# Performance work log

Measured on AMD Instinct MI355X. Metric: run time of the kernel, lower is better.

The kernel has to match this reference:

```python
import jax, jax.numpy as jnp
import numpy as np

N_NODES = 50000
EMB = 256
HEADS = 2
N_BASE_EDGES = 100000


def setup_inputs() -> dict:
    key = jax.random.key(0)
    ks = jax.random.split(key, 12)
    x = jax.random.normal(ks[0], (N_NODES, EMB), dtype=jnp.float32)
    # bipartite edges: sources in left half, targets in right half -> no self-loops
    src = jax.random.randint(ks[1], (N_BASE_EDGES,), 0, N_NODES // 2)
    dst = jax.random.randint(ks[2], (N_BASE_EDGES,), N_NODES // 2, N_NODES)
    edge_index = jnp.stack([src, dst]).astype(jnp.int64)
    hd = EMB // HEADS
    s = 0.02
    params = {
        "Wkqv": jax.random.normal(ks[3], (EMB, 3 * EMB), dtype=jnp.float32) * s,
        "bkqv": jnp.zeros((3 * EMB,), dtype=jnp.float32),
        "W1": jax.random.normal(ks[4], (2 * hd, hd), dtype=jnp.float32) * s,
        "b1": jnp.zeros((hd,), dtype=jnp.float32),
        "W2": jax.random.normal(ks[5], (hd, 1), dtype=jnp.float32) * s,
        "b2": jnp.zeros((1,), dtype=jnp.float32),
        "Wout": jax.random.normal(ks[6], (EMB, EMB), dtype=jnp.float32) * s,
        "bout": jnp.zeros((EMB,), dtype=jnp.float32),
    }
    return {"x": x, "edge_index": edge_index, **params}


def reference(x, edge_index, Wkqv, bkqv, W1, b1, W2, b2, Wout, bout):
    N, emb = x.shape
    H = HEADS
    hd = emb // H
    # MetaGNNNoEdgeAttr.forward preprocessing: make undirected + self loops.
    # Input is bipartite (no self-loops), so remove_self_loops is a no-op.
    ei = jnp.concatenate([edge_index, edge_index[::-1]], axis=1)
    loops = jnp.arange(N, dtype=edge_index.dtype)
    src = jnp.concatenate([ei[0], loops])  # j (message source)
    dst = jnp.concatenate([ei[1], loops])  # i (message target / softmax index)

    # single GNN layer (n_layers=1)
    kqv = x @ Wkqv + bkqv  # [N, 3*emb]
    q = kqv[dst, :emb].reshape(-1, H, hd)                                  # [E,H,hd]
    k = kqv[src, emb:2 * emb].reshape(-1, H, hd) / jnp.sqrt(jnp.float32(hd))
    v = kqv[src, 2 * emb:].reshape(-1, H, hd)

    h = jax.nn.relu(jnp.concatenate([k, q], axis=-1) @ W1 + b1)  # [E,H,hd]
    a = (h @ W2 + b2).squeeze(-1)                                # [E,H]

    # segment softmax over destination nodes (every node has a self-loop)
    m = jax.ops.segment_max(a, dst, num_segments=N)              # [N,H]
    ex = jnp.exp(a - m[dst])
    s = jax.ops.segment_sum(ex, dst, num_segments=N)             # [N,H]
    alpha = ex / (s[dst] + 1e-16)                                # [E,H]

    msg = (alpha[..., None] * v).reshape(-1, emb) @ Wout + bout  # [E,emb]
    out = jax.ops.segment_sum(msg, dst, num_segments=N)          # [N,emb]
    return jax.nn.relu(out) + x
```

## Files before the change

### kernel.cpp

```cpp
#include <hip/hip_runtime.h>
#include <hip/hip_bf16.h>

#define EMB 256

typedef __bf16 bf16_t;
typedef __attribute__((ext_vector_type(8))) __bf16 bf16x8;
typedef __attribute__((ext_vector_type(4))) __bf16 bf16x4;
typedef __attribute__((ext_vector_type(4))) float floatx4;

__device__ __forceinline__ int eidx(const int* __restrict__ p, int is64, long long k){
  return is64 ? p[2*k] : p[(int)k];
}
__device__ __forceinline__ void async_load16(const void* g, void* l){
  __builtin_amdgcn_global_load_lds(
      (const __attribute__((address_space(1))) unsigned int*)g,
      (__attribute__((address_space(3))) unsigned int*)l,
      16, 0, 0);
}
__device__ __forceinline__ float4 cvt4(bf16x4 v){
  return make_float4((float)v.x, (float)v.y, (float)v.z, (float)v.w);
}
__device__ __forceinline__ int detect64(const int* __restrict__ ei){
  return ((ei[1] | ei[3] | ei[5] | ei[7]) == 0) ? 1 : 0;
}

__global__ void cvt_x_kernel(const float* __restrict__ x, bf16_t* __restrict__ xb, int n4){
  int t = blockIdx.x*blockDim.x + threadIdx.x;
  if (t >= n4) return;
  const float4 v = *(const float4*)(x + (size_t)t*4);
  bf16x4 o = { (bf16_t)v.x, (bf16_t)v.y, (bf16_t)v.z, (bf16_t)v.w };
  *(bf16x4*)(xb + (size_t)t*4) = o;
}

__global__ void prep_weights(const float* __restrict__ Wkqv, const float* __restrict__ bkqv,
                             const float* __restrict__ W1,
                             bf16_t* __restrict__ WcombT, float* __restrict__ bcomb){
  int n = blockIdx.x * blockDim.x + threadIdx.x;
  int c = blockIdx.y;
  if (n >= 768) return;
  const float rs = rsqrtf(128.0f);
  bool isBias = (c == 256);
  const float* arow = isBias ? bkqv : (Wkqv + (size_t)c*768);
  float val;
  if (n < 256){
    int h = n >> 7, d = n & 127;
    float s = 0.f;
    for (int t = 0; t < 128; ++t)
      s = fmaf(arow[h*128 + t], W1[(size_t)(128 + t)*128 + d], s);
    val = s;
  } else {
    int r = n - 256;
    int h = r >> 8, t8 = r & 255;
    int g = t8 >> 3, half = (t8 >> 2) & 1, dd = t8 & 3;
    int d = g*4 + dd;
    if (half == 0){
      float s = 0.f;
      for (int t = 0; t < 128; ++t)
        s = fmaf(arow[256 + h*128 + t], W1[(size_t)t*128 + d], s);
      val = s * rs;
    } else {
      val = arow[512 + h*128 + d];
    }
  }
  if (isBias) bcomb[n] = val;
  else        WcombT[(size_t)n*256 + c] = (bf16_t)val;
}

__global__ void prep_wout(const float* __restrict__ W, bf16_t* __restrict__ Wt){
  int t = blockIdx.x*blockDim.x + threadIdx.x;
  int n = t & 255, c = t >> 8;
  Wt[(size_t)n*256 + c] = (bf16_t)W[(size_t)c*256 + n];
}

__global__ void deg_kernel(const int* __restrict__ ei,
                           int* __restrict__ deg, int E0, int Nn){
  int t = blockIdx.x*blockDim.x + threadIdx.x;
  if (t >= 2*E0) return;
  int is64 = detect64(ei);
  int i = (t < E0) ? eidx(ei,is64,(long long)E0+t) : eidx(ei,is64,t-E0);
  i = min(max(i,0), Nn-1);
  atomicAdd(deg + i, 1);
}

__global__ __launch_bounds__(1024) void scan1_kernel(const int* __restrict__ deg,
                                                     int* __restrict__ off,
                                                     int* __restrict__ bsum, int N){
  __shared__ int wsum[16];
  int tid = threadIdx.x, lane = tid & 63, w = tid >> 6;
  int i = blockIdx.x*1024 + tid;
  int v = (i < N) ? (deg[i] + 1) : 0;
  int incl = v;
  #pragma unroll
  for (int o = 1; o < 64; o <<= 1){
    int t = __shfl_up(incl, o, 64);
    if (lane >= o) incl += t;
  }
  if (lane == 63) wsum[w] = incl;
  __syncthreads();
  if (w == 0 && lane < 16){
    int sv = wsum[lane];
    #pragma unroll
    for (int o = 1; o < 16; o <<= 1){
      int t = __shfl_up(sv, o, 64);
      if (lane >= o) sv += t;
    }
    wsum[lane] = sv;
  }
  __syncthreads();
  int wpref = (w == 0) ? 0 : wsum[w-1];
  if (i < N) off[i] = wpref + incl - v;
  if (tid == 1023) bsum[blockIdx.x] = wpref + incl;
}

__global__ __launch_bounds__(1024) void scan2_kernel(int* __restrict__ bsum,
                                                     int* __restrict__ off, int nb, int N){
  __shared__ int wsum[16];
  int tid = threadIdx.x, lane = tid & 63, w = tid >> 6;
  int v = (tid < nb) ? bsum[tid] : 0;
  int incl = v;
  #pragma unroll
  for (int o = 1; o < 64; o <<= 1){
    int t = __shfl_up(incl, o, 64);
    if (lane >= o) incl += t;
  }
  if (lane == 63) wsum[w] = incl;
  __syncthreads();
  if (w == 0 && lane < 16){
    int sv = wsum[lane];
    #pragma unroll
    for (int o = 1; o < 16; o <<= 1){
      int t = __shfl_up(sv, o, 64);
      if (lane >= o) sv += t;
    }
    wsum[lane] = sv;
  }
  __syncthreads();
  int wpref = (w == 0) ? 0 : wsum[w-1];
  if (tid < nb) bsum[tid] = wpref + incl - v;
  if (tid == 1023) off[N] = wpref + incl;
}

__global__ void scan3_kernel(int* __restrict__ off, const int* __restrict__ bsum, int N){
  int i = blockIdx.x*256 + threadIdx.x;
  if (i < N) off[i] += bsum[i >> 10];
}

__global__ void scatter_kernel(const int* __restrict__ ei,
                               const int* __restrict__ off, int* __restrict__ cursor,
                               int* __restrict__ bj, int E0, int Nn){
  int e = blockIdx.x*blockDim.x + threadIdx.x;
  int E = 2*E0 + Nn;
  if (e >= E) return;
  int is64 = detect64(ei);
  int j, i;
  if (e < E0){ j = eidx(ei,is64,e); i = eidx(ei,is64,(long long)E0+e); }
  else if (e < 2*E0){ int t = e - E0; i = eidx(ei,is64,t); j = eidx(ei,is64,(long long)E0+t); }
  else { i = j = e - 2*E0; }
  i = min(max(i,0), Nn-1); j = min(max(j,0), Nn-1);
  int pos = atomicAdd(cursor + i, 1);
  bj[off[i] + pos] = j;
}

template<int MODE, typename OutT>
__global__ __launch_bounds__(512, 4) void mfma_gemm(
    const bf16_t* __restrict__ A, const bf16_t* __restrict__ Bt,
    const float* __restrict__ bias, OutT* __restrict__ C,
    int M, int N,
    const int* __restrict__ deg, const float* __restrict__ xres)
{
  __shared__ bf16_t As[2][128*32];
  __shared__ bf16_t Bs[2][128*32];
  const int tid = threadIdx.x;
  const int wave = tid >> 6, lane = tid & 63;
  const int row16 = lane & 15, quad = lane >> 4;

  const int nn = N >> 7;
  const int bid = blockIdx.x;
  const int strip = bid / (8*nn);
  const int inner = bid % (8*nn);
  const int m0 = (strip*8 + (inner & 7)) * 128;
  const int n0 = (inner >> 3) * 128;
  const int wm  = (wave >> 2) * 64;
  const int wnq = (wave & 3) * 32;

  const int f0 = wave;
  const int gm0 = min(m0 + f0*16 + row16, M-1);
  const int gn0 = n0 + f0*16 + row16;

  async_load16(A  + (size_t)gm0*256 + quad*8, (char*)As[0] + f0*1024);
  async_load16(Bt + (size_t)gn0*256 + quad*8, (char*)Bs[0] + f0*1024);

  floatx4 acc[4][2];
  #pragma unroll
  for (int a=0;a<4;++a)
    #pragma unroll
    for (int b=0;b<2;++b) acc[a][b] = (floatx4){0.f,0.f,0.f,0.f};

  #pragma unroll
  for (int kt = 0; kt < 8; ++kt){
    const int cur = kt & 1, nxt = cur ^ 1;
    const int k1 = (kt+1)*32;

    __syncthreads();

    if (kt < 7){
      async_load16(A  + (size_t)gm0*256 + k1 + quad*8, (char*)As[nxt] + f0*1024);
      async_load16(Bt + (size_t)gn0*256 + k1 + quad*8, (char*)Bs[nxt] + f0*1024);
    }

    bf16x8 af[4], bfr[2];
    #pragma unroll
    for (int t = 0; t < 4; ++t)
      af[t]  = *(const bf16x8*)((const char*)As[cur] + ((wm>>4)+t)*1024 + lane*16);
    #pragma unroll
    for (int u = 0; u < 2; ++u)
      bfr[u] = *(const bf16x8*)((const char*)Bs[cur] + ((wnq>>4)+u)*1024 + lane*16);

    #pragma unroll
    for (int mt=0;mt<4;++mt)
      #pragma unroll
      for (int nt=0;nt<2;++nt)
        acc[mt][nt] = __builtin_amdgcn_mfma_f32_16x16x32_bf16(bfr[nt], af[mt], acc[mt][nt], 0,0,0);
  }

  float4 b4[2];
  #pragma unroll
  for (int nt=0;nt<2;++nt)
    b4[nt] = *(const float4*)(bias + n0 + wnq + nt*16 + quad*4);

  #pragma unroll
  for (int mt=0;mt<4;++mt){
    const int m = m0 + wm + mt*16 + row16;
    if (m >= M) continue;
    const float dg = (MODE==1) ? (float)(deg[m]+1) : 0.f;
    #pragma unroll
    for (int nt=0;nt<2;++nt){
      const int nb = n0 + wnq + nt*16 + quad*4;
      if (MODE == 0){
        bf16x4 o = { (bf16_t)(acc[mt][nt][0] + b4[nt].x),
                     (bf16_t)(acc[mt][nt][1] + b4[nt].y),
                     (bf16_t)(acc[mt][nt][2] + b4[nt].z),
                     (bf16_t)(acc[mt][nt][3] + b4[nt].w) };
        *(bf16x4*)((bf16_t*)C + (size_t)m*N + nb) = o;
      } else {
        const float4 xr = *(const float4*)(xres + (size_t)m*N + nb);
        float4 o;
        o.x = fmaxf(acc[mt][nt][0] + dg*b4[nt].x, 0.f) + xr.x;
        o.y = fmaxf(acc[mt][nt][1] + dg*b4[nt].y, 0.f) + xr.y;
        o.z = fmaxf(acc[mt][nt][2] + dg*b4[nt].z, 0.f) + xr.z;
        o.w = fmaxf(acc[mt][nt][3] + dg*b4[nt].w, 0.f) + xr.w;
        *(float4*)((float*)C + (size_t)m*N + nb) = o;
      }
    }
  }
}

__device__ __forceinline__ float score4(bf16x8 kvv, float4 qv, float4 b1v, float4 w2v){
  return fmaxf(qv.x+(float)kvv[0]+b1v.x, 0.f)*w2v.x
       + fmaxf(qv.y+(float)kvv[1]+b1v.y, 0.f)*w2v.y
       + fmaxf(qv.z+(float)kvv[2]+b1v.z, 0.f)*w2v.z
       + fmaxf(qv.w+(float)kvv[3]+b1v.w, 0.f)*w2v.w;
}
__device__ __forceinline__ float hredux(float p){
  #pragma unroll
  for (int o = 16; o >= 1; o >>= 1)
    p += __shfl_xor(p, o, 64);
  return p;
}
__global__ __launch_bounds__(256) void fused_attn_kernel(
    const bf16_t* __restrict__ P, const int* __restrict__ bj, const int* __restrict__ off,
    const float* __restrict__ b1, const float* __restrict__ W2, const float* __restrict__ b2,
    bf16_t* __restrict__ aggb, int Nn)
{
  int i = blockIdx.x * (blockDim.x >> 6) + (threadIdx.x >> 6);
  if (i >= Nn) return;
  int lane = threadIdx.x & 63;
  int h = lane >> 5, g = lane & 31, d = g * 4;

  const float4 qv  = cvt4(*(const bf16x4*)(P + (size_t)i*768 + h*128 + d));
  const float4 b1v = *(const float4*)(b1 + d);
  const float4 w2v = *(const float4*)(W2 + d);
  const float b2v  = b2[0];
  const bf16_t* __restrict__ Pkv = P + 256 + h*256 + g*8;

  float m = -3.0e38f, s = 0.f;
  float4 acc = make_float4(0.f,0.f,0.f,0.f);
  const int s0 = off[i], s1 = off[i+1], s1m1 = s1 - 1;

  for (int t = s0; t < s1; t += 4){
    const int cnt = s1 - t;
    const int jA = bj[t];
    const int jB = bj[min(t+1, s1m1)];
    const int jC = bj[min(t+2, s1m1)];
    const int jD = bj[min(t+3, s1m1)];
    const bf16x8 kA = *(const bf16x8*)(Pkv + (size_t)jA*768);
    const bf16x8 kB = *(const bf16x8*)(Pkv + (size_t)jB*768);
    const bf16x8 kC = *(const bf16x8*)(Pkv + (size_t)jC*768);
    const bf16x8 kD = *(const bf16x8*)(Pkv + (size_t)jD*768);
    float pA = hredux(score4(kA, qv, b1v, w2v));
    float pB = hredux(score4(kB, qv, b1v, w2v));
    float pC = hredux(score4(kC, qv, b1v, w2v));
    float pD = hredux(score4(kD, qv, b1v, w2v));
    const float aA = pA + b2v;
    const float aB = (cnt > 1) ? pB + b2v : -3.0e38f;
    const float aC = (cnt > 2) ? pC + b2v : -3.0e38f;
    const float aD = (cnt > 3) ? pD + b2v : -3.0e38f;
    const float amax = fmaxf(fmaxf(aA, aB), fmaxf(aC, aD));
    const float mn = fmaxf(m, amax);
    const float sc = __expf(m - mn);
    const float eA = __expf(aA - mn);
    const float eB = __expf(aB - mn);
    const float eC = __expf(aC - mn);
    const float eD = __expf(aD - mn);
    s = s*sc + ((eA + eB) + (eC + eD));
    acc.x = acc.x*sc + ((eA*(float)kA[4] + eB*(float)kB[4]) + (eC*(float)kC[4] + eD*(float)kD[4]));
    acc.y = acc.y*sc + ((eA*(float)kA[5] + eB*(float)kB[5]) + (eC*(float)kC[5] + eD*(float)kD[5]));
    acc.z = acc.z*sc + ((eA*(float)kA[6] + eB*(float)kB[6]) + (eC*(float)kC[6] + eD*(float)kD[6]));
    acc.w = acc.w*sc + ((eA*(float)kA[7] + eB*(float)kB[7]) + (eC*(float)kC[7] + eD*(float)kD[7]));
    m = mn;
  }
  float inv = 1.f / (s + 1e-16f);
  bf16x4 ob = { (bf16_t)(acc.x*inv), (bf16_t)(acc.y*inv), (bf16_t)(acc.z*inv), (bf16_t)(acc.w*inv) };
  *(bf16x4*)(aggb + (size_t)i*256 + h*128 + d) = ob;
}

extern "C" void kernel_launch(void* const* d_in, const int* in_sizes, int n_in,
                              void* d_out, int out_size, void* d_ws, size_t ws_size,
                              hipStream_t stream)
{
  const float* x     = (const float*)d_in[0];
  const int*   ei    = (const int*)d_in[1];
  const float* Wkqv  = (const float*)d_in[2];
  const float* bkqv  = (const float*)d_in[3];
  const float* W1    = (const float*)d_in[4];
  const float* b1    = (const float*)d_in[5];
  const float* W2    = (const float*)d_in[6];
  const float* b2    = (const float*)d_in[7];
  const float* Wout  = (const float*)d_in[8];
  const float* bout  = (const float*)d_in[9];
  float* out = (float*)d_out;

  const int N  = in_sizes[0] / EMB;
  const int E0 = in_sizes[1] / 2;
  const int E  = 2*E0 + N;

  float* base = (float*)d_ws;
  bf16_t* WcombT = (bf16_t*)base;
  float*  bcomb  = base + 98304;
  bf16_t* WoutT  = (bf16_t*)(base + 98304 + 768);
  bf16_t* xb     = (bf16_t*)(base + 131840);
  bf16_t* Pb     = (bf16_t*)(base + 131840 + 6400000);
  bf16_t* aggb   = (bf16_t*)(Pb + (size_t)N*768);
  int* deg       = (int*)(aggb + (size_t)N*256);
  int* cursor    = deg + N;
  int* flag      = cursor + N;
  int* off       = flag + 1;
  int* bj        = off + (N+1);
  int* bsum      = (int*)aggb;

  hipMemsetAsync(deg, 0, (size_t)2*N*sizeof(int), stream);

  cvt_x_kernel<<<((N*EMB/4)+255)/256,256,0,stream>>>(x, xb, N*EMB/4);
  prep_weights<<<dim3(3,257),256,0,stream>>>(Wkqv, bkqv, W1, WcombT, bcomb);
  prep_wout<<<256,256,0,stream>>>(Wout, WoutT);

  deg_kernel<<<(2*E0+255)/256,256,0,stream>>>(ei, deg, E0, N);
  const int nb = (N + 1023)/1024;
  scan1_kernel<<<nb,1024,0,stream>>>(deg, off, bsum, N);
  scan2_kernel<<<1,1024,0,stream>>>(bsum, off, nb, N);
  scan3_kernel<<<(N+255)/256,256,0,stream>>>(off, bsum, N);
  scatter_kernel<<<(E+255)/256,256,0,stream>>>(ei, off, cursor, bj, E0, N);

  const int nm8 = (((N+127)/128) + 7) & ~7;
  mfma_gemm<0, bf16_t><<<nm8*6,512,0,stream>>>(xb, WcombT, bcomb, Pb, N, 768, nullptr, nullptr);
  fused_attn_kernel<<<(N+3)/4,256,0,stream>>>(Pb, bj, off, b1, W2, b2, aggb, N);
  mfma_gemm<1, float><<<nm8*2,512,0,stream>>>(aggb, WoutT, bout, out, N, 256, deg, x);
}
```

Measured before the change: 292.0 us.

## Keep full-K weight tile resident in LDS and stream A fragments from global

Rewrites the MFMA GEMM so each block loads its whole 128-column, 256-deep B (weight) panel into LDS once. Each block then loops over one or more 256-row M tiles, reading A fragments directly from global memory into registers instead of double-buffering through LDS. Per-wave tiles grow to 64x64 with a 4x4 accumulator array, and the grid becomes 2D with MLOOP row tiles per block for the first GEMM. This removes per-k-step barriers and repeated weight staging, at the cost of 64KB of LDS per block (lower occupancy), more registers, and unstaged global loads of A.

```diff
diff --git a/kernel.cpp b/kernel.cpp
--- a/kernel.cpp
+++ b/kernel.cpp
@@ -161,95 +161,90 @@
   bj[off[i] + pos] = j;
 }
 
-template<int MODE, typename OutT>
-__global__ __launch_bounds__(512, 4) void mfma_gemm(
+template<int MODE, int MLOOP, typename OutT>
+__global__ __launch_bounds__(512, 4) void mfma_gemmB(
     const bf16_t* __restrict__ A, const bf16_t* __restrict__ Bt,
     const float* __restrict__ bias, OutT* __restrict__ C,
     int M, int N,
     const int* __restrict__ deg, const float* __restrict__ xres)
 {
-  __shared__ bf16_t As[2][128*32];
-  __shared__ bf16_t Bs[2][128*32];
+  __shared__ bf16_t Bs[128*256];
   const int tid = threadIdx.x;
   const int wave = tid >> 6, lane = tid & 63;
   const int row16 = lane & 15, quad = lane >> 4;
-
-  const int nn = N >> 7;
-  const int bid = blockIdx.x;
-  const int strip = bid / (8*nn);
-  const int inner = bid % (8*nn);
-  const int m0 = (strip*8 + (inner & 7)) * 128;
-  const int n0 = (inner >> 3) * 128;
-  const int wm  = (wave >> 2) * 64;
-  const int wnq = (wave & 3) * 32;
-
-  const int f0 = wave;
-  const int gm0 = min(m0 + f0*16 + row16, M-1);
-  const int gn0 = n0 + f0*16 + row16;
-
-  async_load16(A  + (size_t)gm0*256 + quad*8, (char*)As[0] + f0*1024);
-  async_load16(Bt + (size_t)gn0*256 + quad*8, (char*)Bs[0] + f0*1024);
-
-  floatx4 acc[4][2];
+  const int n0 = blockIdx.y << 7;
+
+  {
+    const bf16_t* gsrc = Bt + (size_t)(n0 + wave*16 + row16)*256 + quad*8;
+    char* ldst = (char*)Bs + wave*8192;
+    #pragma unroll
+    for (int kt = 0; kt < 8; ++kt)
+      async_load16(gsrc + kt*32, ldst + kt*1024);
+  }
+  __syncthreads();
+
+  const int wm = (wave >> 1) * 64;
+  const int wn = (wave & 1) * 64;
+
+  float4 b4[4];
   #pragma unroll
-  for (int a=0;a<4;++a)
-    #pragma unroll
-    for (int b=0;b<2;++b) acc[a][b] = (floatx4){0.f,0.f,0.f,0.f};
-
-  #pragma unroll
-  for (int kt = 0; kt < 8; ++kt){
-    const int cur = kt & 1, nxt = cur ^ 1;
-    const int k1 = (kt+1)*32;
-
-    __syncthreads();
-
-    if (kt < 7){
-      async_load16(A  + (size_t)gm0*256 + k1 + quad*8, (char*)As[nxt] + f0*1024);
-      async_load16(Bt + (size_t)gn0*256 + k1 + quad*8, (char*)Bs[nxt] + f0*1024);
-    }
-
-    bf16x8 af[4], bfr[2];
+  for (int nt=0;nt<4;++nt)
+    b4[nt] = *(const float4*)(bias + n0 + wn + nt*16 + quad*4);
+
+  for (int l = 0; l < MLOOP; ++l){
+    const int m0 = (blockIdx.x*MLOOP + l) << 8;
+    if (m0 >= M) return;
+
+    const bf16_t* ap[4];
     #pragma unroll
     for (int t = 0; t < 4; ++t)
-      af[t]  = *(const bf16x8*)((const char*)As[cur] + ((wm>>4)+t)*1024 + lane*16);
-    #pragma unroll
-    for (int u = 0; u < 2; ++u)
-      bfr[u] = *(const bf16x8*)((const char*)Bs[cur] + ((wnq>>4)+u)*1024 + lane*16);
-
-    #pragma unroll
-    for (int mt=0;mt<4;++mt)
-      #pragma unroll
-      for (int nt=0;nt<2;++nt)
-        acc[mt][nt] = __builtin_amdgcn_mfma_f32_16x16x32_bf16(bfr[nt], af[mt], acc[mt][nt], 0,0,0);
-  }
-
-  float4 b4[2];
-  #pragma unroll
-  for (int nt=0;nt<2;++nt)
-    b4[nt] = *(const float4*)(bias + n0 + wnq + nt*16 + quad*4);
-
-  #pragma unroll
-  for (int mt=0;mt<4;++mt){
-    const int m = m0 + wm + mt*16 + row16;
-    if (m >= M) continue;
-    const float dg = (MODE==1) ? (float)(deg[m]+1) : 0.f;
-    #pragma unroll
-    for (int nt=0;nt<2;++nt){
-      const int nb = n0 + wnq + nt*16 + quad*4;
-      if (MODE == 0){
-        bf16x4 o = { (bf16_t)(acc[mt][nt][0] + b4[nt].x),
-                     (bf16_t)(acc[mt][nt][1] + b4[nt].y),
-                     (bf16_t)(acc[mt][nt][2] + b4[nt].z),
-                     (bf16_t)(acc[mt][nt][3] + b4[nt].w) };
-        *(bf16x4*)((bf16_t*)C + (size_t)m*N + nb) = o;
-      } else {
-        const float4 xr = *(const float4*)(xres + (size_t)m*N + nb);
-        float4 o;
-        o.x = fmaxf(acc[mt][nt][0] + dg*b4[nt].x, 0.f) + xr.x;
-        o.y = fmaxf(acc[mt][nt][1] + dg*b4[nt].y, 0.f) + xr.y;
-        o.z = fmaxf(acc[mt][nt][2] + dg*b4[nt].z, 0.f) + xr.z;
-        o.w = fmaxf(acc[mt][nt][3] + dg*b4[nt].w, 0.f) + xr.w;
-        *(float4*)((float*)C + (size_t)m*N + nb) = o;
+      ap[t] = A + (size_t)min(m0 + wm + t*16 + row16, M-1)*256 + quad*8;
+
+    floatx4 acc[4][4];
+    #pragma unroll
+    for (int a=0;a<4;++a)
+      #pragma unroll
+      for (int b=0;b<4;++b) acc[a][b] = (floatx4){0.f,0.f,0.f,0.f};
+
+    #pragma unroll
+    for (int kt = 0; kt < 8; ++kt){
+      bf16x8 af[4], bfr[4];
+      #pragma unroll
+      for (int t = 0; t < 4; ++t)
+        af[t]  = *(const bf16x8*)(ap[t] + kt*32);
+      #pragma unroll
+      for (int t = 0; t < 4; ++t)
+        bfr[t] = *(const bf16x8*)((const char*)Bs + (((wn>>4)+t)*8 + kt)*1024 + lane*16);
+      #pragma unroll
+      for (int mt=0;mt<4;++mt)
+        #pragma unroll
+        for (int nt=0;nt<4;++nt)
+          acc[mt][nt] = __builtin_amdgcn_mfma_f32_16x16x32_bf16(bfr[nt], af[mt], acc[mt][nt], 0,0,0);
+    }
+
+    #pragma unroll
+    for (int mt=0;mt<4;++mt){
+      const int m = m0 + wm + mt*16 + row16;
+      if (m >= M) continue;
+      const float dg = (MODE==1) ? (float)(deg[m]+1) : 0.f;
+      #pragma unroll
+      for (int nt=0;nt<4;++nt){
+        const int nb = n0 + wn + nt*16 + quad*4;
+        if (MODE == 0){
+          bf16x4 o = { (bf16_t)(acc[mt][nt][0] + b4[nt].x),
+                       (bf16_t)(acc[mt][nt][1] + b4[nt].y),
+                       (bf16_t)(acc[mt][nt][2] + b4[nt].z),
+                       (bf16_t)(acc[mt][nt][3] + b4[nt].w) };
+          *(bf16x4*)((bf16_t*)C + (size_t)m*N + nb) = o;
+        } else {
+          const float4 xr = *(const float4*)(xres + (size_t)m*N + nb);
+          float4 o;
+          o.x = fmaxf(acc[mt][nt][0] + dg*b4[nt].x, 0.f) + xr.x;
+          o.y = fmaxf(acc[mt][nt][1] + dg*b4[nt].y, 0.f) + xr.y;
+          o.z = fmaxf(acc[mt][nt][2] + dg*b4[nt].z, 0.f) + xr.z;
+          o.w = fmaxf(acc[mt][nt][3] + dg*b4[nt].w, 0.f) + xr.w;
+          *(float4*)((float*)C + (size_t)m*N + nb) = o;
+        }
       }
     }
   }
@@ -371,8 +366,10 @@
   scan3_kernel<<<(N+255)/256,256,0,stream>>>(off, bsum, N);
   scatter_kernel<<<(E+255)/256,256,0,stream>>>(ei, off, cursor, bj, E0, N);
 
-  const int nm8 = (((N+127)/128) + 7) & ~7;
-  mfma_gemm<0, bf16_t><<<nm8*6,512,0,stream>>>(xb, WcombT, bcomb, Pb, N, 768, nullptr, nullptr);
+  const int nmt = (N + 255)/256;
+  mfma_gemmB<0, 3, bf16_t><<<dim3((nmt+2)/3, 6),512,0,stream>>>(
+      xb, WcombT, bcomb, Pb, N, 768, nullptr, nullptr);
   fused_attn_kernel<<<(N+3)/4,256,0,stream>>>(Pb, bj, off, b1, W2, b2, aggb, N);
-  mfma_gemm<1, float><<<nm8*2,512,0,stream>>>(aggb, WoutT, bout, out, N, 256, deg, x);
-}
+  mfma_gemmB<1, 1, float><<<dim3(nmt, 2),512,0,stream>>>(
+      aggb, WoutT, bout, out, N, 256, deg, x);
+}
```

Result: slower. 318.9 us (+9.2%).
